# Kernel optimization log

Measured on AMD Instinct MI355X. Metric: run time of the kernel, lower is better.

Reference implementation:

```python
import jax, jax.numpy as jnp
import numpy as np

NUM_QUBITS = 8
QD = 2 ** NUM_QUBITS          # 256
PI = float(np.pi)
D_MODEL = 512
NUM_HEADS = 8
HEAD_DIM = D_MODEL // NUM_HEADS
LN_EPS = 1e-5


def _superposition(feat):
    # torch bug faithfully reproduced: state starts as e0 and is *multiplied*
    # by per-qubit amplitudes, so only index 0 survives. All values real.
    B, S, d = feat.shape
    idx = np.arange(NUM_QUBITS) % d
    theta = feat[:, :, idx] * PI                       # [B,S,nq]
    cos_h = jnp.cos(theta * 0.5)
    sin_h = jnp.sin(theta * 0.5)
    mask = (np.arange(QD)[None, :] >> np.arange(NUM_QUBITS)[:, None]) & 1  # [nq,QD]
    amps = jnp.where(mask[None, None] == 0, cos_h[..., None], sin_h[..., None])  # [B,S,nq,QD]
    prod = jnp.prod(amps, axis=2)                      # [B,S,QD]
    e0 = jnp.zeros((QD,), feat.dtype).at[0].set(1.0)
    state = prod * e0
    norm = jnp.sqrt(jnp.sum(state * state, axis=-1, keepdims=True))
    return state / (norm + 1e-10)


def _linear_entangle(ent):
    # entangle_matrix is block-diagonal with symmetric 2x2 blocks [[a,a],[a,-a]];
    # state @ M.T == pairwise 2x2 matmul (identical math, avoids 65536^2 matrix)
    B, S, D = ent.shape
    a = 0.7071
    M = jnp.array([[a, a], [a, -a]], ent.dtype)
    return (ent.reshape(B, S, D // 2, 2) @ M).reshape(B, S, D)


def _layer_norm(x, g, b):
    m = jnp.mean(x, axis=-1, keepdims=True)
    v = jnp.mean((x - m) ** 2, axis=-1, keepdims=True)
    return (x - m) * jax.lax.rsqrt(v + LN_EPS) * g + b


def setup_inputs() -> dict:
    key = jax.random.key(0)
    ks = jax.random.split(key, 16)
    D = D_MODEL
    s = 1.0 / np.sqrt(D)
    inp = {
        'audio_features': jax.random.normal(ks[0], (2, 256, D), jnp.float32),
        'visual_features': jax.random.normal(ks[1], (2, 256, D), jnp.float32),
        'Wq': jax.random.normal(ks[2], (D, D), jnp.float32) * s,
        'bq': jnp.zeros((D,), jnp.float32),
        'Wk': jax.random.normal(ks[3], (D, D), jnp.float32) * s,
        'bk': jnp.zeros((D,), jnp.float32),
        'Wv': jax.random.normal(ks[4], (D, D), jnp.float32) * s,
        'bv': jnp.zeros((D,), jnp.float32),
        'Wo': jax.random.normal(ks[5], (D, D), jnp.float32) * s,
        'bo': jnp.zeros((D,), jnp.float32),
        'We': jax.random.normal(ks[6], (D, D), jnp.float32) * s,
        'be': jnp.zeros((D,), jnp.float32),
        'gamma': jnp.ones((D,), jnp.float32),
        'beta': jnp.zeros((D,), jnp.float32),
    }
    return inp


def reference(audio_features, visual_features, Wq, bq, Wk, bk, Wv, bv,
              Wo, bo, We, be, gamma, beta):
    B, S, D = audio_features.shape
    H, hd = NUM_HEADS, HEAD_DIM

    aq = audio_features @ Wq + bq
    av = audio_features @ Wv + bv
    vk = visual_features @ Wk + bk
    vv = visual_features @ Wv + bv

    qa = _superposition(audio_features @ We + be)    # [B,S,QD]
    qv = _superposition(visual_features @ We + be)   # [B,S,QD]
    ent = (qa[..., :, None] * qv[..., None, :]).reshape(B, S, QD * QD)
    ent = _linear_entangle(ent)                      # [B,S,QD^2]

    probs = ent * ent
    qsum = jnp.sum(probs, axis=-1)                   # [B,S]
    ang = jnp.where(ent < 0, PI, 0.0)                # angle of a real number
    interference = jnp.cos(jnp.mean(ang, axis=-1))   # [B,S]
    scale = (qsum * interference)[:, None, :, None]  # [B,1,S,1]

    def heads(x):
        return x.reshape(B, S, H, hd).transpose(0, 2, 1, 3)

    aqh, vkh, vvh, avh = heads(aq), heads(vk), heads(vv), heads(av)
    logits = scale * jnp.einsum('bhqd,bhkd->bhqk', aqh, vkh) / np.sqrt(hd)
    attn = jax.nn.softmax(logits, axis=-1)           # [B,H,S,S]

    audio_att = jnp.einsum('bhqk,bhkd->bhqd', attn, vvh)
    visual_att = jnp.einsum('bhqk,bhqd->bhkd', attn, avh)
    audio_out = audio_att.transpose(0, 2, 1, 3).reshape(B, S, D) @ Wo + bo
    visual_out = visual_att.transpose(0, 2, 1, 3).reshape(B, S, D) @ Wo + bo

    audio_final = _layer_norm(audio_features + audio_out, gamma, beta)
    visual_final = _layer_norm(visual_features + visual_out, gamma, beta)

    quantum_coherence = jnp.mean(jnp.abs(ent))
    pn = probs / (jnp.sum(probs, axis=-1, keepdims=True) + 1e-10)
    entanglement_entropy = jnp.mean(-jnp.sum(pn * jnp.log(pn + 1e-10), axis=-1))

    return (audio_final, visual_final, quantum_coherence,
            entanglement_entropy, attn[:, -1])
```

## Files before the change

### kernel.cpp

```cpp
#include <hip/hip_runtime.h>
#include <math.h>

#define PI_F 3.14159265358979323846f

typedef __attribute__((ext_vector_type(8))) short short8v;
typedef __attribute__((ext_vector_type(4))) float f32x4;
typedef __attribute__((ext_vector_type(16))) float f32x16;

__device__ __forceinline__ unsigned short f2bf(float f) {
    unsigned int u = __float_as_uint(f);
    u += 0x7fffu + ((u >> 16) & 1u);
    return (unsigned short)(u >> 16);
}

__device__ __forceinline__ unsigned int cvtpk_bf16(float lo, float hi) {
    unsigned int r;
    asm("v_cvt_pk_bf16_f32 %0, %1, %2" : "=v"(r) : "v"(lo), "v"(hi));
    return r;
}

union W8 { unsigned int w[4]; short8v v; };

__device__ __forceinline__ void gload_lds16(const void* g, void* l) {
    __builtin_amdgcn_global_load_lds((const __attribute__((address_space(1))) unsigned int*)g,
                                     (__attribute__((address_space(3))) unsigned int*)l, 16, 0, 0);
}

__global__ __launch_bounds__(256) void prep_tok(const float* __restrict__ audio,
                                                const float* __restrict__ visual,
                                                const float* __restrict__ Wq,
                                                const float* __restrict__ Wk,
                                                const float* __restrict__ Wv,
                                                const float* __restrict__ Wo,
                                                const float* __restrict__ We,
                                                const float* __restrict__ be,
                                                unsigned short* __restrict__ audio_b,
                                                unsigned short* __restrict__ visual_b,
                                                unsigned short* __restrict__ Wqt,
                                                unsigned short* __restrict__ Wkt,
                                                unsigned short* __restrict__ Wvt,
                                                unsigned short* __restrict__ Wot,
                                                float* __restrict__ scale,
                                                float* __restrict__ coh_tok,
                                                float* __restrict__ ent_tok) {
    __shared__ float tile[32][33];
    const int bid = blockIdx.x;
    if (bid < 1536) {
        const int z = bid >> 8;
        const int x0 = (bid & 15) * 32, y0 = ((bid >> 4) & 15) * 32;
        const int tx = threadIdx.x & 31, ty = threadIdx.x >> 5;
        if (z < 2) {
            const float* src = z ? visual : audio;
            unsigned short* dst = z ? visual_b : audio_b;
#pragma unroll
            for (int i = 0; i < 4; i++) {
                int r = y0 + ty + i * 8;
                dst[r * 512 + x0 + tx] = f2bf(src[r * 512 + x0 + tx]);
            }
        } else {
            const float* src = (z == 2) ? Wq : (z == 3) ? Wk : (z == 4) ? Wv : Wo;
            unsigned short* dst = (z == 2) ? Wqt : (z == 3) ? Wkt : (z == 4) ? Wvt : Wot;
#pragma unroll
            for (int i = 0; i < 4; i++)
                tile[ty + i * 8][tx] = src[(y0 + ty + i * 8) * 512 + x0 + tx];
            __syncthreads();
#pragma unroll
            for (int i = 0; i < 4; i++) {
                int n = x0 + ty + i * 8;
                dst[n * 512 + y0 + tx] = f2bf(tile[tx][ty + i * 8]);
            }
        }
    } else {
        const int t = (bid - 1536) * 4 + (threadIdx.x >> 6);
        const int lane = threadIdx.x & 63;
        float accA[8] = {}, accV[8] = {};
#pragma unroll
        for (int i = 0; i < 8; i++) {
            int k = i * 64 + lane;
            float wa = audio[t * 512 + k], wv = visual[t * 512 + k];
            const float* wrow = &We[k * 512];
#pragma unroll
            for (int c = 0; c < 8; c++) {
                float w = wrow[c];
                accA[c] += wa * w;
                accV[c] += wv * w;
            }
        }
#pragma unroll
        for (int c = 0; c < 8; c++) {
#pragma unroll
            for (int o = 32; o >= 1; o >>= 1) {
                accA[c] += __shfl_xor(accA[c], o);
                accV[c] += __shfl_xor(accV[c], o);
            }
        }
        if (lane == 0) {
            float pa = 1.f, pv = 1.f;
#pragma unroll
            for (int c = 0; c < 8; c++) {
                pa *= cosf((accA[c] + be[c]) * (PI_F * 0.5f));
                pv *= cosf((accV[c] + be[c]) * (PI_F * 0.5f));
            }
            float s0a = pa / (fabsf(pa) + 1e-10f);
            float s0v = pv / (fabsf(pv) + 1e-10f);
            float e = s0a * s0v;
            const float a = 0.7071f;
            float ent0 = a * e;
            float qsum = 2.f * ent0 * ent0;
            float interf = (ent0 < 0.f) ? cosf(2.f * PI_F / 65536.f) : 1.f;
            scale[t] = qsum * interf;
            coh_tok[t] = 2.f * fabsf(ent0);
            float p = (ent0 * ent0) / (qsum + 1e-10f);
            ent_tok[t] = -2.f * p * logf(p + 1e-10f);
        }
    }
}

struct MfmaArgs {
    const unsigned short* A[4];
    const unsigned short* Bt[4];
    const float* bias[4];
    void* C[4];
    int obf[4];
    int otr[4];
};

__global__ __launch_bounds__(256) void gemm_mfma(MfmaArgs args) {
    const int zb = blockIdx.z;
    const unsigned short* __restrict__ A = args.A[zb];
    const unsigned short* __restrict__ Bt = args.Bt[zb];
    const float* __restrict__ bias = args.bias[zb];
    const int otr = args.otr[zb];

    const int n0 = blockIdx.x * 64;
    const int m0 = blockIdx.y * 64;

    __shared__ unsigned short As[64 * 128];
    __shared__ unsigned short Bs[64 * 128];

    const int tid = threadIdx.x;
    const int lane = tid & 63;
    const int wid = tid >> 6;
    const int wr = wid >> 1, wc = wid & 1;
    const int l15 = lane & 15;
    const int lhi = lane >> 4;

    const int sRow = tid >> 4;
    const int lcS = (tid & 15) ^ (sRow & 15);

    f32x4 acc[2][2] = {};

    for (int kt = 0; kt < 4; kt++) {
        const int k0 = kt * 128;
#pragma unroll
        for (int i = 0; i < 4; i++) {
            int r = i * 16 + sRow;
            gload_lds16(A + (size_t)(m0 + r) * 512 + k0 + lcS * 8,
                        (char*)As + i * 4096 + wid * 1024);
            gload_lds16(Bt + (size_t)(n0 + r) * 512 + k0 + lcS * 8,
                        (char*)Bs + i * 4096 + wid * 1024);
        }
        __syncthreads();
#pragma unroll
        for (int ks = 0; ks < 4; ks++) {
            short8v a[2], b[2];
            const int lcr = ks * 4 + lhi;
#pragma unroll
            for (int qi = 0; qi < 2; qi++) {
                int row = wr * 32 + qi * 16 + l15;
                int slot = lcr ^ (row & 15);
                a[qi] = *(const short8v*)((const char*)As + row * 256 + slot * 16);
            }
#pragma unroll
            for (int nj = 0; nj < 2; nj++) {
                int row = wc * 32 + nj * 16 + l15;
                int slot = lcr ^ (row & 15);
                b[nj] = *(const short8v*)((const char*)Bs + row * 256 + slot * 16);
            }
            if (otr) {
#pragma unroll
                for (int qi = 0; qi < 2; qi++)
#pragma unroll
                    for (int nj = 0; nj < 2; nj++)
                        acc[qi][nj] = __builtin_amdgcn_mfma_f32_16x16x32_bf16(b[nj], a[qi], acc[qi][nj], 0, 0, 0);
            } else {
#pragma unroll
                for (int qi = 0; qi < 2; qi++)
#pragma unroll
                    for (int nj = 0; nj < 2; nj++)
                        acc[qi][nj] = __builtin_amdgcn_mfma_f32_16x16x32_bf16(a[qi], b[nj], acc[qi][nj], 0, 0, 0);
            }
        }
        __syncthreads();
    }

    if (otr) {
        unsigned short* __restrict__ Ct = (unsigned short*)args.C[zb];
#pragma unroll
        for (int qi = 0; qi < 2; qi++)
#pragma unroll
            for (int nj = 0; nj < 2; nj++)
#pragma unroll
                for (int r = 0; r < 4; r++) {
                    int nrow = n0 + wc * 32 + nj * 16 + lhi * 4 + r;
                    int tcol = m0 + wr * 32 + qi * 16 + l15;
                    Ct[nrow * 512 + tcol] = f2bf(acc[qi][nj][r] + bias[nrow]);
                }
    } else if (args.obf[zb]) {
        unsigned short* __restrict__ Cb = (unsigned short*)args.C[zb];
#pragma unroll
        for (int qi = 0; qi < 2; qi++)
#pragma unroll
            for (int nj = 0; nj < 2; nj++)
#pragma unroll
                for (int r = 0; r < 4; r++) {
                    int row = m0 + wr * 32 + qi * 16 + lhi * 4 + r;
                    int col = n0 + wc * 32 + nj * 16 + l15;
                    Cb[row * 512 + col] = f2bf(acc[qi][nj][r] + bias[col]);
                }
    } else {
        float* __restrict__ C = (float*)args.C[zb];
#pragma unroll
        for (int qi = 0; qi < 2; qi++)
#pragma unroll
            for (int nj = 0; nj < 2; nj++)
#pragma unroll
                for (int r = 0; r < 4; r++) {
                    int row = m0 + wr * 32 + qi * 16 + lhi * 4 + r;
                    int col = n0 + wc * 32 + nj * 16 + l15;
                    C[row * 512 + col] = acc[qi][nj][r] + bias[col];
                }
    }
}

__global__ __launch_bounds__(512, 2) void attn_roles(const unsigned short* __restrict__ aqb,
                                                     const unsigned short* __restrict__ vkb,
                                                     const unsigned short* __restrict__ vvt,
                                                     const unsigned short* __restrict__ avt,
                                                     const float* __restrict__ scale,
                                                     const float* __restrict__ coh,
                                                     const float* __restrict__ entt,
                                                     unsigned short* __restrict__ attcat_b,
                                                     float* __restrict__ attn_last,
                                                     float* __restrict__ scal_out) {
    __shared__ char smem[65536];
    char* Kb = smem;
    char* VF = smem + 32768;

    const int tid = threadIdx.x;
    const int wid = tid >> 6;
    const int lane = tid & 63;
    const int lq = lane & 31;
    const int hi = lane >> 5;

    if (blockIdx.x == 8) {
        if (blockIdx.y || blockIdx.z) return;
        float c = coh[tid], e = entt[tid];
#pragma unroll
        for (int o = 32; o >= 1; o >>= 1) {
            c += __shfl_xor(c, o);
            e += __shfl_xor(e, o);
        }
        float* rc = (float*)smem;
        float* re = rc + 8;
        if (lane == 0) { rc[wid] = c; re[wid] = e; }
        __syncthreads();
        if (tid == 0) {
            float cs = 0.f, es = 0.f;
#pragma unroll
            for (int i = 0; i < 8; i++) { cs += rc[i]; es += re[i]; }
            scal_out[0] = cs / (512.f * 65536.f);
            scal_out[1] = es / 512.f;
        }
        return;
    }

    const int h = blockIdx.x, b = blockIdx.y, role = blockIdx.z;

    {
#pragma unroll
        for (int i = 0; i < 4; i++) {
            int r = wid * 32 + i * 8 + (lane >> 3);
            int lc = (lane & 7) ^ (r & 7);
            gload_lds16(vkb + (size_t)(b * 256 + r) * 512 + h * 64 + lc * 8,
                        Kb + wid * 4096 + i * 1024);
        }
    }

    if (role == 0) {
#pragma unroll
        for (int i = 0; i < 4; i++) {
            gload_lds16(vvt + (size_t)(h * 64 + 32 * hi + lq) * 512 + b * 256 + 32 * wid + 8 * i,
                        VF + wid * 4096 + i * 1024);
        }
    }
    __syncthreads();

    f32x16 p[8] = {};
    {
        short8v qf[4];
        const unsigned short* qbase = aqb + (size_t)(b * 256 + wid * 32 + lq) * 512 + h * 64;
#pragma unroll
        for (int s = 0; s < 4; s++) qf[s] = *(const short8v*)(qbase + (2 * s + hi) * 8);
#pragma unroll
        for (int t = 0; t < 8; t++) {
            const int krow = t * 32 + lq;
#pragma unroll
            for (int s = 0; s < 4; s++) {
                int slot = (2 * s + hi) ^ (krow & 7);
                short8v kf = *(const short8v*)(Kb + krow * 128 + (slot << 4));
                p[t] = __builtin_amdgcn_mfma_f32_32x32x16_bf16(kf, qf[s], p[t], 0, 0, 0);
            }
        }
    }

    {
        const float sq = scale[b * 256 + wid * 32 + lq] * 0.125f;
        float mx = -1e30f;
#pragma unroll
        for (int t = 0; t < 8; t++) {
            p[t] *= sq;
#pragma unroll
            for (int r = 0; r < 16; r++) mx = fmaxf(mx, p[t][r]);
        }
        mx = fmaxf(mx, __shfl_xor(mx, 32));
        float sum = 0.f;
#pragma unroll
        for (int t = 0; t < 8; t++)
#pragma unroll
            for (int r = 0; r < 16; r++) {
                float e = __expf(p[t][r] - mx);
                p[t][r] = e;
                sum += e;
            }
        sum += __shfl_xor(sum, 32);
        float inv = 1.0f / sum;
#pragma unroll
        for (int t = 0; t < 8; t++) p[t] *= inv;
    }

    if (role == 0) {
        f32x16 aacc[2] = {};
#pragma unroll
        for (int t = 0; t < 8; t++) {
            unsigned int c0 = cvtpk_bf16(p[t][0], p[t][1]);
            unsigned int c1 = cvtpk_bf16(p[t][2], p[t][3]);
            unsigned int c2 = cvtpk_bf16(p[t][4], p[t][5]);
            unsigned int c3 = cvtpk_bf16(p[t][6], p[t][7]);
            unsigned int e0 = (unsigned int)__shfl_xor((int)c0, 32);
            unsigned int e1 = (unsigned int)__shfl_xor((int)c1, 32);
            unsigned int e2 = (unsigned int)__shfl_xor((int)c2, 32);
            unsigned int e3 = (unsigned int)__shfl_xor((int)c3, 32);
            W8 fa0;
            fa0.w[0] = hi ? e2 : c0;
            fa0.w[1] = hi ? e3 : c1;
            fa0.w[2] = hi ? c2 : e0;
            fa0.w[3] = hi ? c3 : e1;
            unsigned int c4 = cvtpk_bf16(p[t][8], p[t][9]);
            unsigned int c5 = cvtpk_bf16(p[t][10], p[t][11]);
            unsigned int c6 = cvtpk_bf16(p[t][12], p[t][13]);
            unsigned int c7 = cvtpk_bf16(p[t][14], p[t][15]);
            unsigned int e4 = (unsigned int)__shfl_xor((int)c4, 32);
            unsigned int e5 = (unsigned int)__shfl_xor((int)c5, 32);
            unsigned int e6 = (unsigned int)__shfl_xor((int)c6, 32);
            unsigned int e7 = (unsigned int)__shfl_xor((int)c7, 32);
            W8 fa1;
            fa1.w[0] = hi ? e6 : c4;
            fa1.w[1] = hi ? e7 : c5;
            fa1.w[2] = hi ? c6 : e4;
            fa1.w[3] = hi ? c7 : e5;
#pragma unroll
            for (int dt = 0; dt < 2; dt++) {
                short8v vf = *(const short8v*)(VF + ((((t * 4 + hi) * 2 + dt) * 32 + lq) << 4));
                aacc[dt] = __builtin_amdgcn_mfma_f32_32x32x16_bf16(fa0.v, vf, aacc[dt], 0, 0, 0);
                short8v vg = *(const short8v*)(VF + ((((t * 4 + hi + 2) * 2 + dt) * 32 + lq) << 4));
                aacc[dt] = __builtin_amdgcn_mfma_f32_32x32x16_bf16(fa1.v, vg, aacc[dt], 0, 0, 0);
            }
        }
#pragma unroll
        for (int dt = 0; dt < 2; dt++)
#pragma unroll
            for (int r = 0; r < 16; r++) {
                int qrow = wid * 32 + (r & 3) + 8 * (r >> 2) + 4 * hi;
                attcat_b[(size_t)(b * 256 + qrow) * 512 + h * 64 + 32 * dt + lq] = f2bf(aacc[dt][r]);
            }
        __syncthreads();

        if (h == 7) {
            float* tile = (float*)smem + (size_t)wid * (32 * 33);
            const int q2 = lane >> 1, koff = (lane & 1) * 16;
#pragma unroll
            for (int t = 0; t < 8; t++) {
#pragma unroll
                for (int r = 0; r < 16; r++)
                    tile[lq * 33 + ((r & 3) + 8 * (r >> 2) + 4 * hi)] = p[t][r];
                float* orow = attn_last + (size_t)(b * 256 + wid * 32 + q2) * 256 + 32 * t + koff;
#pragma unroll
                for (int j = 0; j < 16; j++) orow[j] = tile[q2 * 33 + koff + j];
            }
        }
        return;
    }

    __syncthreads();

    {
#pragma unroll
        for (int i = 0; i < 4; i++) {
            gload_lds16(avt + (size_t)(h * 64 + 32 * hi + lq) * 512 + b * 256 + 8 * (wid * 4 + i),
                        Kb + wid * 4096 + i * 1024);
        }
        if ((wid >> 1) == 0) {
            const int dq = (wid & 1) * 32 + lq;
#pragma unroll
            for (int t = 0; t < 8; t++)
#pragma unroll
                for (int r = 0; r < 16; r++) {
                    int k = 32 * t + (r & 3) + 8 * (r >> 2) + 4 * hi;
                    int slot = (dq >> 3) ^ ((k ^ (k >> 3)) & 7);
                    *(unsigned short*)(VF + k * 128 + slot * 16 + (dq & 7) * 2) = f2bf(p[t][r]);
                }
        }
    }
    __syncthreads();

    f32x16 vacc[2] = {};
    {
        const int krow = wid * 32 + lq;
        const int xr = (krow ^ (krow >> 3)) & 7;
#pragma unroll
        for (int c = 0; c < 4; c++) {
#pragma unroll
            for (int uc = 0; uc < 4; uc++) {
                int slot = (2 * uc + hi) ^ xr;
                short8v pa = *(const short8v*)(VF + krow * 128 + slot * 16);
                int m = 2 * (4 * c + uc) + hi;
#pragma unroll
                for (int dt = 0; dt < 2; dt++) {
                    short8v af = *(const short8v*)(Kb + (((m * 2 + dt) * 32 + lq) << 4));
                    vacc[dt] = __builtin_amdgcn_mfma_f32_32x32x16_bf16(pa, af, vacc[dt], 0, 0, 0);
                }
            }
            if (c < 3) {
                __syncthreads();
                if ((wid >> 1) == c + 1) {
                    const int dq = (wid & 1) * 32 + lq;
#pragma unroll
                    for (int t = 0; t < 8; t++)
#pragma unroll
                        for (int r = 0; r < 16; r++) {
                            int k = 32 * t + (r & 3) + 8 * (r >> 2) + 4 * hi;
                            int slot = (dq >> 3) ^ ((k ^ (k >> 3)) & 7);
                            *(unsigned short*)(VF + k * 128 + slot * 16 + (dq & 7) * 2) = f2bf(p[t][r]);
                        }
                }
                __syncthreads();
            }
        }
    }
#pragma unroll
    for (int dt = 0; dt < 2; dt++)
#pragma unroll
        for (int r = 0; r < 16; r++) {
            int krow = wid * 32 + (r & 3) + 8 * (r >> 2) + 4 * hi;
            attcat_b[(size_t)(512 + b * 256 + krow) * 512 + h * 64 + 32 * dt + lq] = f2bf(vacc[dt][r]);
        }
}

__global__ __launch_bounds__(256) void ln_final(const float* __restrict__ xa,
                                                const float* __restrict__ xv,
                                                const float* __restrict__ proj,
                                                const float* __restrict__ gamma,
                                                const float* __restrict__ beta,
                                                float* __restrict__ out) {
    __shared__ float red[4];
    const int t = blockIdx.x;
    const int tid = threadIdx.x;
    const int wid = tid >> 6, lane = tid & 63;

    const float* x = (t < 512) ? (xa + t * 512) : (xv + (t - 512) * 512);
    const float* pp = proj + t * 512;

    float y0 = x[tid] + pp[tid];
    float y1 = x[tid + 256] + pp[tid + 256];

    float s = y0 + y1;
#pragma unroll
    for (int o = 32; o >= 1; o >>= 1) s += __shfl_xor(s, o);
    if (lane == 0) red[wid] = s;
    __syncthreads();
    float mean = (red[0] + red[1] + red[2] + red[3]) * (1.f / 512.f);

    float d0 = y0 - mean, d1 = y1 - mean;
    float v = d0 * d0 + d1 * d1;
    __syncthreads();
#pragma unroll
    for (int o = 32; o >= 1; o >>= 1) v += __shfl_xor(v, o);
    if (lane == 0) red[wid] = v;
    __syncthreads();
    float var = (red[0] + red[1] + red[2] + red[3]) * (1.f / 512.f);
    float rstd = rsqrtf(var + 1e-5f);

    out[t * 512 + tid] = d0 * rstd * gamma[tid] + beta[tid];
    out[t * 512 + tid + 256] = d1 * rstd * gamma[tid + 256] + beta[tid + 256];
}

extern "C" void kernel_launch(void* const* d_in, const int* in_sizes, int n_in,
                              void* d_out, int out_size, void* d_ws, size_t ws_size,
                              hipStream_t stream) {
    const float* audio  = (const float*)d_in[0];
    const float* visual = (const float*)d_in[1];
    const float* Wq = (const float*)d_in[2];
    const float* bq = (const float*)d_in[3];
    const float* Wk = (const float*)d_in[4];
    const float* bk = (const float*)d_in[5];
    const float* Wv = (const float*)d_in[6];
    const float* bv = (const float*)d_in[7];
    const float* Wo = (const float*)d_in[8];
    const float* bo = (const float*)d_in[9];
    const float* We = (const float*)d_in[10];
    const float* be = (const float*)d_in[11];
    const float* gamma = (const float*)d_in[12];
    const float* beta  = (const float*)d_in[13];
    float* out = (float*)d_out;

    float* ws = (float*)d_ws;
    float* proj  = ws;
    float* scale = ws + 524288;
    float* coh   = ws + 524800;
    float* entt  = ws + 525312;
    unsigned short* attcat_b = (unsigned short*)(ws + 525824);
    unsigned short* audio_b  = (unsigned short*)(ws + 787968);
    unsigned short* visual_b = (unsigned short*)(ws + 919040);
    unsigned short* Wqt  = (unsigned short*)(ws + 1050112);
    unsigned short* Wkt  = (unsigned short*)(ws + 1181184);
    unsigned short* Wvt  = (unsigned short*)(ws + 1312256);
    unsigned short* Wot  = (unsigned short*)(ws + 1443328);
    unsigned short* aq_b = (unsigned short*)(ws + 1574400);
    unsigned short* vk_b = (unsigned short*)(ws + 1705472);
    unsigned short* vvt  = (unsigned short*)(ws + 1836544);
    unsigned short* avt  = (unsigned short*)(ws + 1967616);

    hipLaunchKernelGGL(prep_tok, dim3(1664), dim3(256), 0, stream,
                       audio, visual, Wq, Wk, Wv, Wo, We, be,
                       audio_b, visual_b, Wqt, Wkt, Wvt, Wot,
                       scale, coh, entt);

    MfmaArgs g1;
    g1.A[0] = audio_b;  g1.Bt[0] = Wqt; g1.bias[0] = bq; g1.C[0] = aq_b; g1.obf[0] = 1; g1.otr[0] = 0;
    g1.A[1] = visual_b; g1.Bt[1] = Wkt; g1.bias[1] = bk; g1.C[1] = vk_b; g1.obf[1] = 1; g1.otr[1] = 0;
    g1.A[2] = visual_b; g1.Bt[2] = Wvt; g1.bias[2] = bv; g1.C[2] = vvt;  g1.obf[2] = 1; g1.otr[2] = 1;
    g1.A[3] = audio_b;  g1.Bt[3] = Wvt; g1.bias[3] = bv; g1.C[3] = avt;  g1.obf[3] = 1; g1.otr[3] = 1;
    hipLaunchKernelGGL(gemm_mfma, dim3(8, 8, 4), dim3(256), 0, stream, g1);

    hipLaunchKernelGGL(attn_roles, dim3(9, 2, 2), dim3(512), 0, stream,
                       aq_b, vk_b, vvt, avt, scale, coh, entt,
                       attcat_b, out + 524290, out + 524288);

    MfmaArgs g2;
    for (int i = 0; i < 4; i++) {
        g2.A[i] = attcat_b; g2.Bt[i] = Wot; g2.bias[i] = bo; g2.C[i] = proj;
        g2.obf[i] = 0; g2.otr[i] = 0;
    }
    hipLaunchKernelGGL(gemm_mfma, dim3(8, 16, 1), dim3(256), 0, stream, g2);

    hipLaunchKernelGGL(ln_final, dim3(1024), dim3(256), 0, stream,
                       audio, visual, proj, gamma, beta, out);
}
```

Baseline: 49.69 us.

## Shrink GEMM tiles to 32x32 and load full K panel in one pass

The MFMA GEMM drops from 64x64 output tiles with a 4-step K loop to 32x32 tiles. Each block now loads the whole K=512 panel into LDS at once with an XOR swizzle, and each wave computes a single 16x16 accumulator. Grids grow 4x so the small GEMMs fill more compute units, and the mid-loop barrier is removed. In exchange there is less operand reuse per block, more total global traffic, and more LDS per block (64KB), which can limit occupancy.

```diff
diff --git a/kernel.cpp b/kernel.cpp
--- a/kernel.cpp
+++ b/kernel.cpp
@@ -132,11 +132,11 @@
     const float* __restrict__ bias = args.bias[zb];
     const int otr = args.otr[zb];
 
-    const int n0 = blockIdx.x * 64;
-    const int m0 = blockIdx.y * 64;
-
-    __shared__ unsigned short As[64 * 128];
-    __shared__ unsigned short Bs[64 * 128];
+    const int n0 = blockIdx.x * 32;
+    const int m0 = blockIdx.y * 32;
+
+    __shared__ unsigned short As[32 * 512];
+    __shared__ unsigned short Bs[32 * 512];
 
     const int tid = threadIdx.x;
     const int lane = tid & 63;
@@ -145,91 +145,55 @@
     const int l15 = lane & 15;
     const int lhi = lane >> 4;
 
-    const int sRow = tid >> 4;
-    const int lcS = (tid & 15) ^ (sRow & 15);
-
-    f32x4 acc[2][2] = {};
-
-    for (int kt = 0; kt < 4; kt++) {
-        const int k0 = kt * 128;
-#pragma unroll
-        for (int i = 0; i < 4; i++) {
-            int r = i * 16 + sRow;
-            gload_lds16(A + (size_t)(m0 + r) * 512 + k0 + lcS * 8,
-                        (char*)As + i * 4096 + wid * 1024);
-            gload_lds16(Bt + (size_t)(n0 + r) * 512 + k0 + lcS * 8,
-                        (char*)Bs + i * 4096 + wid * 1024);
-        }
-        __syncthreads();
-#pragma unroll
-        for (int ks = 0; ks < 4; ks++) {
-            short8v a[2], b[2];
-            const int lcr = ks * 4 + lhi;
-#pragma unroll
-            for (int qi = 0; qi < 2; qi++) {
-                int row = wr * 32 + qi * 16 + l15;
-                int slot = lcr ^ (row & 15);
-                a[qi] = *(const short8v*)((const char*)As + row * 256 + slot * 16);
-            }
-#pragma unroll
-            for (int nj = 0; nj < 2; nj++) {
-                int row = wc * 32 + nj * 16 + l15;
-                int slot = lcr ^ (row & 15);
-                b[nj] = *(const short8v*)((const char*)Bs + row * 256 + slot * 16);
-            }
-            if (otr) {
-#pragma unroll
-                for (int qi = 0; qi < 2; qi++)
-#pragma unroll
-                    for (int nj = 0; nj < 2; nj++)
-                        acc[qi][nj] = __builtin_amdgcn_mfma_f32_16x16x32_bf16(b[nj], a[qi], acc[qi][nj], 0, 0, 0);
-            } else {
-#pragma unroll
-                for (int qi = 0; qi < 2; qi++)
-#pragma unroll
-                    for (int nj = 0; nj < 2; nj++)
-                        acc[qi][nj] = __builtin_amdgcn_mfma_f32_16x16x32_bf16(a[qi], b[nj], acc[qi][nj], 0, 0, 0);
-            }
-        }
-        __syncthreads();
+#pragma unroll
+    for (int i = 0; i < 8; i++) {
+        int row = i * 4 + wid;
+        int lc = lane ^ row;
+        gload_lds16(A + (size_t)(m0 + row) * 512 + lc * 8,
+                    (char*)As + row * 1024);
+        gload_lds16(Bt + (size_t)(n0 + row) * 512 + lc * 8,
+                    (char*)Bs + row * 1024);
+    }
+    __syncthreads();
+
+    f32x4 acc = {};
+    const int arow = wr * 16 + l15;
+    const int brow = wc * 16 + l15;
+#pragma unroll
+    for (int ks = 0; ks < 16; ks++) {
+        const int lcr = ks * 4 + lhi;
+        short8v a = *(const short8v*)((const char*)As + arow * 1024 + ((lcr ^ arow) << 4));
+        short8v b = *(const short8v*)((const char*)Bs + brow * 1024 + ((lcr ^ brow) << 4));
+        if (otr)
+            acc = __builtin_amdgcn_mfma_f32_16x16x32_bf16(b, a, acc, 0, 0, 0);
+        else
+            acc = __builtin_amdgcn_mfma_f32_16x16x32_bf16(a, b, acc, 0, 0, 0);
     }
 
     if (otr) {
         unsigned short* __restrict__ Ct = (unsigned short*)args.C[zb];
 #pragma unroll
-        for (int qi = 0; qi < 2; qi++)
-#pragma unroll
-            for (int nj = 0; nj < 2; nj++)
-#pragma unroll
-                for (int r = 0; r < 4; r++) {
-                    int nrow = n0 + wc * 32 + nj * 16 + lhi * 4 + r;
-                    int tcol = m0 + wr * 32 + qi * 16 + l15;
-                    Ct[nrow * 512 + tcol] = f2bf(acc[qi][nj][r] + bias[nrow]);
-                }
+        for (int r = 0; r < 4; r++) {
+            int nrow = n0 + wc * 16 + lhi * 4 + r;
+            int tcol = m0 + wr * 16 + l15;
+            Ct[nrow * 512 + tcol] = f2bf(acc[r] + bias[nrow]);
+        }
     } else if (args.obf[zb]) {
         unsigned short* __restrict__ Cb = (unsigned short*)args.C[zb];
 #pragma unroll
-        for (int qi = 0; qi < 2; qi++)
-#pragma unroll
-            for (int nj = 0; nj < 2; nj++)
-#pragma unroll
-                for (int r = 0; r < 4; r++) {
-                    int row = m0 + wr * 32 + qi * 16 + lhi * 4 + r;
-                    int col = n0 + wc * 32 + nj * 16 + l15;
-                    Cb[row * 512 + col] = f2bf(acc[qi][nj][r] + bias[col]);
-                }
+        for (int r = 0; r < 4; r++) {
+            int row = m0 + wr * 16 + lhi * 4 + r;
+            int col = n0 + wc * 16 + l15;
+            Cb[row * 512 + col] = f2bf(acc[r] + bias[col]);
+        }
     } else {
         float* __restrict__ C = (float*)args.C[zb];
 #pragma unroll
-        for (int qi = 0; qi < 2; qi++)
-#pragma unroll
-            for (int nj = 0; nj < 2; nj++)
-#pragma unroll
-                for (int r = 0; r < 4; r++) {
-                    int row = m0 + wr * 32 + qi * 16 + lhi * 4 + r;
-                    int col = n0 + wc * 32 + nj * 16 + l15;
-                    C[row * 512 + col] = acc[qi][nj][r] + bias[col];
-                }
+        for (int r = 0; r < 4; r++) {
+            int row = m0 + wr * 16 + lhi * 4 + r;
+            int col = n0 + wc * 16 + l15;
+            C[row * 512 + col] = acc[r] + bias[col];
+        }
     }
 }
 
@@ -551,7 +515,7 @@
     g1.A[1] = visual_b; g1.Bt[1] = Wkt; g1.bias[1] = bk; g1.C[1] = vk_b; g1.obf[1] = 1; g1.otr[1] = 0;
     g1.A[2] = visual_b; g1.Bt[2] = Wvt; g1.bias[2] = bv; g1.C[2] = vvt;  g1.obf[2] = 1; g1.otr[2] = 1;
     g1.A[3] = audio_b;  g1.Bt[3] = Wvt; g1.bias[3] = bv; g1.C[3] = avt;  g1.obf[3] = 1; g1.otr[3] = 1;
-    hipLaunchKernelGGL(gemm_mfma, dim3(8, 8, 4), dim3(256), 0, stream, g1);
+    hipLaunchKernelGGL(gemm_mfma, dim3(16, 16, 4), dim3(256), 0, stream, g1);
 
     hipLaunchKernelGGL(attn_roles, dim3(9, 2, 2), dim3(512), 0, stream,
                        aq_b, vk_b, vvt, avt, scale, coh, entt,
@@ -562,7 +526,7 @@
         g2.A[i] = attcat_b; g2.Bt[i] = Wot; g2.bias[i] = bo; g2.C[i] = proj;
         g2.obf[i] = 0; g2.otr[i] = 0;
     }
-    hipLaunchKernelGGL(gemm_mfma, dim3(8, 16, 1), dim3(256), 0, stream, g2);
+    hipLaunchKernelGGL(gemm_mfma, dim3(16, 32, 1), dim3(256), 0, stream, g2);
 
     hipLaunchKernelGGL(ln_final, dim3(1024), dim3(256), 0, stream,
                        audio, visual, proj, gamma, beta, out);
```

Result: faster. 48.19 us (-3.0%).
